# Kernel optimization log

Hardware: AMD Instinct MI355X
Metric: run time of the kernel (lower is better)

Reference implementation:

```python
import jax, jax.numpy as jnp
import numpy as np

DIM = 768
HEADS = 12
HEAD_DIM = DIM // HEADS
SCALE = HEAD_DIM ** -0.5


def setup_inputs() -> dict:
    key = jax.random.key(0)
    ks = jax.random.split(key, 7)
    B, N, C = 4, 1024, DIM
    s = 0.02
    return {
        "x": jax.random.normal(ks[0], (B, N, C), dtype=jnp.float32),
        "attn_mask": jax.random.normal(ks[1], (B, N, N), dtype=jnp.float32) * 0.1,
        "w_qkv": jax.random.normal(ks[2], (3 * C, C), dtype=jnp.float32) * s,
        "w_proj": jax.random.normal(ks[3], (C, C), dtype=jnp.float32) * s,
        "b_proj": jnp.zeros((C,), dtype=jnp.float32),
        "w_pre": jax.random.normal(ks[4], (HEADS, HEADS), dtype=jnp.float32) * 0.2,
        "w_post": jax.random.normal(ks[5], (HEADS, HEADS), dtype=jnp.float32) * 0.2,
    }


def reference(x, attn_mask, w_qkv, w_proj, b_proj, w_pre, w_post):
    B, N, C = x.shape
    H, D = HEADS, HEAD_DIM
    qkv = (x @ w_qkv.T).reshape(B, N, 3, H, D)
    q, k, v = jnp.moveaxis(qkv, 2, 0)          # each [B, N, H, D]
    q = q.transpose(0, 2, 1, 3)                # [B, H, N, D]
    k = k.transpose(0, 2, 1, 3)
    v = v.transpose(0, 2, 1, 3)
    attn = jnp.einsum("bhnd,bhmd->bhnm", q, k) * SCALE
    attn = attn + attn_mask[:, None, :, :]
    # talking-heads pre-softmax mixing: Linear over head axis (y = x @ W.T)
    attn = jnp.einsum("bhnm,gh->bgnm", attn, w_pre)
    attn = jax.nn.softmax(attn, axis=-1)
    # talking-heads post-softmax mixing
    attn = jnp.einsum("bhnm,gh->bgnm", attn, w_post)
    out = jnp.einsum("bhnm,bhmd->bhnd", attn, v)   # [B, H, N, D]
    out = out.transpose(0, 2, 1, 3).reshape(B, N, C)
    return out @ w_proj.T + b_proj
```

## Files before the change

### kernel.cpp

```cpp
#include <hip/hip_runtime.h>
#include <hip/hip_bf16.h>

typedef __attribute__((ext_vector_type(8))) short bf16x8;
typedef __attribute__((ext_vector_type(4))) float f32x4;
typedef unsigned short u16;

#define ATT_SCALE 0.125f

__device__ __forceinline__ u16 f2bf(float f){
  __hip_bfloat16 h = __float2bfloat16(f);
  return *reinterpret_cast<u16*>(&h);
}
__device__ __forceinline__ float bf2f(u16 u){
  __hip_bfloat16 h;
  *reinterpret_cast<u16*>(&h) = u;
  return __bfloat162float(h);
}

__global__ __launch_bounds__(256) void cvt_kernel(const float* __restrict__ src,
                                                  u16* __restrict__ dst, int n4){
  int i = blockIdx.x*256 + threadIdx.x;
  if (i < n4){
    float4 v = reinterpret_cast<const float4*>(src)[i];
    ushort4 o;
    o.x = f2bf(v.x); o.y = f2bf(v.y); o.z = f2bf(v.z); o.w = f2bf(v.w);
    reinterpret_cast<ushort4*>(dst)[i] = o;
  }
}

template<int BM, int BN, int MODE>
__global__ __launch_bounds__(256) void gemm_bt(
    const u16* __restrict__ A, const u16* __restrict__ B,
    void* __restrict__ C0, void* __restrict__ C1, void* __restrict__ C2,
    const float* __restrict__ bias,
    int M, int N, int K, int lda, int ldb, long sA, long sB, long sC)
{
  constexpr int BK = 32, LDT = 40;
  __shared__ u16 As[BM*LDT];
  __shared__ u16 Bs[BN*LDT];
  const int z = blockIdx.z;
  const u16* Ab = A + (long)z * sA;
  const u16* Bb = B + (long)z * sB;
  const int bm = blockIdx.x * BM, bn = blockIdx.y * BN;
  const int tid = threadIdx.x, lane = tid & 63, wv = tid >> 6;
  constexpr int WM = BM/2, WN = BN/2, FM = WM/16, FN = WN/16;
  const int wm = (wv >> 1) * WM, wn = (wv & 1) * WN;
  const int quad = lane >> 4, cl = lane & 15;
  f32x4 acc[FM][FN];
  #pragma unroll
  for (int i=0;i<FM;i++)
    #pragma unroll
    for (int j=0;j<FN;j++){ f32x4 zr = {0.f,0.f,0.f,0.f}; acc[i][j] = zr; }
  constexpr int AIT = (BM*BK)/(8*256);
  constexpr int BIT = (BN*BK)/(8*256);

  for (int kb = 0; kb < K; kb += BK){
    __syncthreads();
    #pragma unroll
    for (int sL=0; sL<AIT; sL++){
      int e = tid + sL*256, r = e >> 2, c8 = (e & 3) * 8;
      *reinterpret_cast<float4*>(&As[r*LDT + c8]) =
        *reinterpret_cast<const float4*>(Ab + (long)(bm + r)*lda + kb + c8);
    }
    #pragma unroll
    for (int sL=0; sL<BIT; sL++){
      int e = tid + sL*256, r = e >> 2, c8 = (e & 3) * 8;
      *reinterpret_cast<float4*>(&Bs[r*LDT + c8]) =
        *reinterpret_cast<const float4*>(Bb + (long)(bn + r)*ldb + kb + c8);
    }
    __syncthreads();
    bf16x8 af[FM], bfr[FN];
    #pragma unroll
    for (int i=0;i<FM;i++)
      af[i] = *reinterpret_cast<const bf16x8*>(&As[(wm + i*16 + cl)*LDT + quad*8]);
    #pragma unroll
    for (int j=0;j<FN;j++)
      bfr[j] = *reinterpret_cast<const bf16x8*>(&Bs[(wn + j*16 + cl)*LDT + quad*8]);
    #pragma unroll
    for (int i=0;i<FM;i++)
      #pragma unroll
      for (int j=0;j<FN;j++)
        acc[i][j] = __builtin_amdgcn_mfma_f32_16x16x32_bf16(af[i], bfr[j], acc[i][j], 0, 0, 0);
  }

  #pragma unroll
  for (int i=0;i<FM;i++)
  #pragma unroll
  for (int j=0;j<FN;j++)
  #pragma unroll
  for (int r=0;r<4;r++){
    int gm = bm + wm + i*16 + quad*4 + r;
    int gn = bn + wn + j*16 + cl;
    float v = acc[i][j][r];
    if (MODE == 0){
      int b_ = gm >> 10, n_ = gm & 1023;
      int t3 = (gn >= 1536) ? 2 : ((gn >= 768) ? 1 : 0);
      int rem = gn - t3*768;
      int h = rem >> 6, d = rem & 63;
      u16 hv = f2bf(v);
      if (t3 == 0)      ((u16*)C0)[((long)((b_*12 + h)*1024 + n_))*64 + d] = hv;
      else if (t3 == 1) ((u16*)C1)[((long)((b_*12 + h)*1024 + n_))*64 + d] = hv;
      else              ((u16*)C2)[((long)((b_*12 + h)*64 + d))*1024 + n_] = hv;
    } else if (MODE == 1){
      ((u16*)C0)[(long)z*sC + (long)gm*N + gn] = f2bf(v);
    } else if (MODE == 2){
      int b_ = z / 12, h = z - b_*12;
      ((u16*)C0)[((long)((b_*1024 + gm)*12 + h))*64 + gn] = f2bf(v);
    } else {
      ((float*)C0)[(long)gm*N + gn] = v + bias[gn];
    }
  }
}

__global__ __launch_bounds__(256) void mix_kernel(
    u16* __restrict__ S, const float* __restrict__ mask,
    const float* __restrict__ w_pre, const float* __restrict__ w_post)
{
  const int bid = blockIdx.x;
  const int b = bid >> 10, n = bid & 1023;
  const int t = threadIdx.x, wv = t >> 6, lane = t & 63;
  const int m0 = t * 4;

  float s[12][4];
  #pragma unroll
  for (int h=0; h<12; h++){
    ushort4 v = *reinterpret_cast<const ushort4*>(
        S + ((long)((b*12 + h)*1024 + n))*1024 + m0);
    s[h][0]=bf2f(v.x); s[h][1]=bf2f(v.y); s[h][2]=bf2f(v.z); s[h][3]=bf2f(v.w);
  }
  float4 mk = *reinterpret_cast<const float4*>(mask + ((long)(b*1024 + n))*1024 + m0);
  float mkv[4] = {mk.x, mk.y, mk.z, mk.w};

  float smix[12][4];
  #pragma unroll
  for (int g=0; g<12; g++){
    float rs = 0.f;
    #pragma unroll
    for (int h=0; h<12; h++) rs += w_pre[g*12 + h];
    #pragma unroll
    for (int mi=0; mi<4; mi++) smix[g][mi] = rs * mkv[mi];
    #pragma unroll
    for (int h=0; h<12; h++){
      float w = w_pre[g*12 + h] * ATT_SCALE;
      #pragma unroll
      for (int mi=0; mi<4; mi++) smix[g][mi] += w * s[h][mi];
    }
  }

  __shared__ float redA[12][4];
  __shared__ float redB[12][4];
  float Mg[12];
  #pragma unroll
  for (int g=0; g<12; g++){
    float v = fmaxf(fmaxf(smix[g][0], smix[g][1]), fmaxf(smix[g][2], smix[g][3]));
    #pragma unroll
    for (int off=32; off>0; off>>=1) v = fmaxf(v, __shfl_xor(v, off));
    if (lane == 0) redA[g][wv] = v;
  }
  __syncthreads();
  #pragma unroll
  for (int g=0; g<12; g++)
    Mg[g] = fmaxf(fmaxf(redA[g][0], redA[g][1]), fmaxf(redA[g][2], redA[g][3]));

  #pragma unroll
  for (int g=0; g<12; g++){
    float sum = 0.f;
    #pragma unroll
    for (int mi=0; mi<4; mi++){
      float e = __expf(smix[g][mi] - Mg[g]);
      smix[g][mi] = e; sum += e;
    }
    #pragma unroll
    for (int off=32; off>0; off>>=1) sum += __shfl_xor(sum, off);
    if (lane == 0) redB[g][wv] = sum;
  }
  __syncthreads();
  #pragma unroll
  for (int g=0; g<12; g++){
    float L = redB[g][0] + redB[g][1] + redB[g][2] + redB[g][3];
    float inv = 1.f / L;
    #pragma unroll
    for (int mi=0; mi<4; mi++) smix[g][mi] *= inv;
  }

  #pragma unroll
  for (int h=0; h<12; h++){
    float o0=0.f,o1=0.f,o2=0.f,o3=0.f;
    #pragma unroll
    for (int g=0; g<12; g++){
      float w = w_post[h*12 + g];
      o0 += w*smix[g][0]; o1 += w*smix[g][1]; o2 += w*smix[g][2]; o3 += w*smix[g][3];
    }
    ushort4 st; st.x=f2bf(o0); st.y=f2bf(o1); st.z=f2bf(o2); st.w=f2bf(o3);
    *reinterpret_cast<ushort4*>(S + ((long)((b*12 + h)*1024 + n))*1024 + m0) = st;
  }
}

extern "C" void kernel_launch(void* const* d_in, const int* in_sizes, int n_in,
                              void* d_out, int out_size, void* d_ws, size_t ws_size,
                              hipStream_t stream)
{
  const float* x      = (const float*)d_in[0];
  const float* mask   = (const float*)d_in[1];
  const float* w_qkv  = (const float*)d_in[2];
  const float* w_proj = (const float*)d_in[3];
  const float* b_proj = (const float*)d_in[4];
  const float* w_pre  = (const float*)d_in[5];
  const float* w_post = (const float*)d_in[6];
  float* out = (float*)d_out;

  u16* xb     = (u16*)d_ws;
  u16* wqkvb  = xb     + 4096l*768;
  u16* wprojb = wqkvb  + 2304l*768;
  u16* Qb     = wprojb + 768l*768;
  u16* Kb     = Qb     + 48l*1024*64;
  u16* Vtb    = Kb     + 48l*1024*64;
  u16* tmpb   = Vtb    + 48l*1024*64;
  u16* Sb     = tmpb   + 4096l*768;
  size_t need = ((size_t)(Sb - xb) + 48ul*1024*1024) * sizeof(u16);
  if (ws_size < need) return;

  cvt_kernel<<<(4096*768/4 + 255)/256, 256, 0, stream>>>(x,      xb,     4096*768/4);
  cvt_kernel<<<(2304*768/4 + 255)/256, 256, 0, stream>>>(w_qkv,  wqkvb,  2304*768/4);
  cvt_kernel<<<(768*768/4  + 255)/256, 256, 0, stream>>>(w_proj, wprojb, 768*768/4);

  dim3 gq(4096/128, 2304/128, 1);
  gemm_bt<128,128,0><<<gq, 256, 0, stream>>>(xb, wqkvb, Qb, Kb, Vtb, nullptr,
      4096, 2304, 768, 768, 768, 0, 0, 0);

  dim3 gs(1024/128, 1024/128, 48);
  gemm_bt<128,128,1><<<gs, 256, 0, stream>>>(Qb, Kb, Sb, nullptr, nullptr, nullptr,
      1024, 1024, 64, 64, 64, 1024l*64, 1024l*64, 1024l*1024);

  mix_kernel<<<4096, 256, 0, stream>>>(Sb, mask, w_pre, w_post);

  dim3 gp(1024/128, 1, 48);
  gemm_bt<128,64,2><<<gp, 256, 0, stream>>>(Sb, Vtb, tmpb, nullptr, nullptr, nullptr,
      1024, 64, 1024, 1024, 1024, 1024l*1024, 64l*1024, 0);

  dim3 go(4096/128, 768/128, 1);
  gemm_bt<128,128,3><<<go, 256, 0, stream>>>(tmpb, wprojb, out, nullptr, nullptr, b_proj,
      4096, 768, 768, 768, 768, 0, 0, 0);
}
```

Before: 275.3 us.

## Shrink mix kernel to one wave per row, fold scale into weights, merge conversions

The talking-heads mix kernel now runs one 64-thread wave per query row, with each lane handling 16 columns through 16-byte loads and stores. This removes the LDS reductions and __syncthreads, leaving only wave shuffles. The attention scale is folded into the Q part of w_qkv during bf16 conversion, and the three conversion launches are merged into one kernel. The risks are heavy register pressure from the 12x16 accumulator array and fewer threads per block, which could lower occupancy or cause spills.

```diff
diff --git a/kernel.cpp b/kernel.cpp
--- a/kernel.cpp
+++ b/kernel.cpp
@@ -2,10 +2,9 @@
 #include <hip/hip_bf16.h>
 
 typedef __attribute__((ext_vector_type(8))) short bf16x8;
+typedef __attribute__((ext_vector_type(8))) short s16x8;
 typedef __attribute__((ext_vector_type(4))) float f32x4;
 typedef unsigned short u16;
-
-#define ATT_SCALE 0.125f
 
 __device__ __forceinline__ u16 f2bf(float f){
   __hip_bfloat16 h = __float2bfloat16(f);
@@ -17,15 +16,24 @@
   return __bfloat162float(h);
 }
 
-__global__ __launch_bounds__(256) void cvt_kernel(const float* __restrict__ src,
-                                                  u16* __restrict__ dst, int n4){
+__global__ __launch_bounds__(256) void cvt3_kernel(
+    const float* __restrict__ s0, u16* __restrict__ d0, int n0,
+    const float* __restrict__ s1, u16* __restrict__ d1, int n1,
+    const float* __restrict__ s2, u16* __restrict__ d2, int n2)
+{
   int i = blockIdx.x*256 + threadIdx.x;
-  if (i < n4){
-    float4 v = reinterpret_cast<const float4*>(src)[i];
-    ushort4 o;
-    o.x = f2bf(v.x); o.y = f2bf(v.y); o.z = f2bf(v.z); o.w = f2bf(v.w);
-    reinterpret_cast<ushort4*>(dst)[i] = o;
-  }
+  const float* s; u16* d; int idx; float sc = 1.f;
+  if (i < n0){ s = s0; d = d0; idx = i; }
+  else if (i < n0 + n1){
+    idx = i - n0; s = s1; d = d1;
+    if (idx < 768*192) sc = 0.125f;
+  } else if (i < n0 + n1 + n2){
+    idx = i - n0 - n1; s = s2; d = d2;
+  } else return;
+  float4 v = reinterpret_cast<const float4*>(s)[idx];
+  ushort4 o;
+  o.x = f2bf(v.x*sc); o.y = f2bf(v.y*sc); o.z = f2bf(v.z*sc); o.w = f2bf(v.w*sc);
+  reinterpret_cast<ushort4*>(d)[idx] = o;
 }
 
 template<int BM, int BN, int MODE>
@@ -112,87 +120,127 @@
   }
 }
 
-__global__ __launch_bounds__(256) void mix_kernel(
+__global__ __launch_bounds__(64, 2) void mix_kernel(
     u16* __restrict__ S, const float* __restrict__ mask,
     const float* __restrict__ w_pre, const float* __restrict__ w_post)
 {
   const int bid = blockIdx.x;
   const int b = bid >> 10, n = bid & 1023;
-  const int t = threadIdx.x, wv = t >> 6, lane = t & 63;
-  const int m0 = t * 4;
-
-  float s[12][4];
+  const int l = threadIdx.x;
+  const long base0 = (((long)(b*12))*1024 + n) * 1024;
+  const int off0 = l*8, off1 = 512 + l*8;
+
+  float smix[12][16];
+
   #pragma unroll
   for (int h=0; h<12; h++){
-    ushort4 v = *reinterpret_cast<const ushort4*>(
-        S + ((long)((b*12 + h)*1024 + n))*1024 + m0);
-    s[h][0]=bf2f(v.x); s[h][1]=bf2f(v.y); s[h][2]=bf2f(v.z); s[h][3]=bf2f(v.w);
-  }
-  float4 mk = *reinterpret_cast<const float4*>(mask + ((long)(b*1024 + n))*1024 + m0);
-  float mkv[4] = {mk.x, mk.y, mk.z, mk.w};
-
-  float smix[12][4];
-  #pragma unroll
-  for (int g=0; g<12; g++){
-    float rs = 0.f;
-    #pragma unroll
-    for (int h=0; h<12; h++) rs += w_pre[g*12 + h];
-    #pragma unroll
-    for (int mi=0; mi<4; mi++) smix[g][mi] = rs * mkv[mi];
-    #pragma unroll
-    for (int h=0; h<12; h++){
-      float w = w_pre[g*12 + h] * ATT_SCALE;
-      #pragma unroll
-      for (int mi=0; mi<4; mi++) smix[g][mi] += w * s[h][mi];
-    }
-  }
-
-  __shared__ float redA[12][4];
-  __shared__ float redB[12][4];
-  float Mg[12];
-  #pragma unroll
-  for (int g=0; g<12; g++){
-    float v = fmaxf(fmaxf(smix[g][0], smix[g][1]), fmaxf(smix[g][2], smix[g][3]));
-    #pragma unroll
-    for (int off=32; off>0; off>>=1) v = fmaxf(v, __shfl_xor(v, off));
-    if (lane == 0) redA[g][wv] = v;
-  }
-  __syncthreads();
-  #pragma unroll
-  for (int g=0; g<12; g++)
-    Mg[g] = fmaxf(fmaxf(redA[g][0], redA[g][1]), fmaxf(redA[g][2], redA[g][3]));
-
-  #pragma unroll
-  for (int g=0; g<12; g++){
+    const u16* sr = S + base0 + (long)h*1024*1024;
+    bf16x8 v0 = *reinterpret_cast<const bf16x8*>(sr + off0);
+    bf16x8 v1 = *reinterpret_cast<const bf16x8*>(sr + off1);
+    float sv[16];
+    #pragma unroll
+    for (int j=0;j<8;j++){ sv[j] = bf2f((u16)v0[j]); sv[8+j] = bf2f((u16)v1[j]); }
+    if (h == 0){
+      #pragma unroll
+      for (int g=0;g<12;g++){
+        float w = w_pre[g*12];
+        #pragma unroll
+        for (int mi=0;mi<16;mi++) smix[g][mi] = w * sv[mi];
+      }
+    } else {
+      #pragma unroll
+      for (int g=0;g<12;g++){
+        float w = w_pre[g*12 + h];
+        #pragma unroll
+        for (int mi=0;mi<16;mi++) smix[g][mi] += w * sv[mi];
+      }
+    }
+  }
+
+  {
+    const float* mr = mask + ((long)(b*1024 + n))*1024;
+    float mk[16];
+    float4 a0 = *reinterpret_cast<const float4*>(mr + off0);
+    float4 a1 = *reinterpret_cast<const float4*>(mr + off0 + 4);
+    float4 b0 = *reinterpret_cast<const float4*>(mr + off1);
+    float4 b1 = *reinterpret_cast<const float4*>(mr + off1 + 4);
+    mk[0]=a0.x; mk[1]=a0.y; mk[2]=a0.z; mk[3]=a0.w;
+    mk[4]=a1.x; mk[5]=a1.y; mk[6]=a1.z; mk[7]=a1.w;
+    mk[8]=b0.x; mk[9]=b0.y; mk[10]=b0.z; mk[11]=b0.w;
+    mk[12]=b1.x; mk[13]=b1.y; mk[14]=b1.z; mk[15]=b1.w;
+    #pragma unroll
+    for (int g=0;g<12;g++){
+      float rs = 0.f;
+      #pragma unroll
+      for (int h=0;h<12;h++) rs += w_pre[g*12 + h];
+      #pragma unroll
+      for (int mi=0;mi<16;mi++) smix[g][mi] += rs * mk[mi];
+    }
+  }
+
+  float M[12];
+  #pragma unroll
+  for (int g=0;g<12;g++){
+    float a = fmaxf(smix[g][0], smix[g][1]);
+    float c = fmaxf(smix[g][2], smix[g][3]);
+    float e = fmaxf(smix[g][4], smix[g][5]);
+    float f = fmaxf(smix[g][6], smix[g][7]);
+    float a2 = fmaxf(smix[g][8], smix[g][9]);
+    float c2 = fmaxf(smix[g][10], smix[g][11]);
+    float e2 = fmaxf(smix[g][12], smix[g][13]);
+    float f2 = fmaxf(smix[g][14], smix[g][15]);
+    M[g] = fmaxf(fmaxf(fmaxf(a,c), fmaxf(e,f)), fmaxf(fmaxf(a2,c2), fmaxf(e2,f2)));
+  }
+  #pragma unroll
+  for (int off=32; off>0; off>>=1)
+    #pragma unroll
+    for (int g=0;g<12;g++) M[g] = fmaxf(M[g], __shfl_xor(M[g], off));
+
+  float L[12];
+  #pragma unroll
+  for (int g=0;g<12;g++){
     float sum = 0.f;
     #pragma unroll
-    for (int mi=0; mi<4; mi++){
-      float e = __expf(smix[g][mi] - Mg[g]);
+    for (int mi=0;mi<16;mi++){
+      float e = __expf(smix[g][mi] - M[g]);
       smix[g][mi] = e; sum += e;
     }
-    #pragma unroll
-    for (int off=32; off>0; off>>=1) sum += __shfl_xor(sum, off);
-    if (lane == 0) redB[g][wv] = sum;
-  }
-  __syncthreads();
-  #pragma unroll
-  for (int g=0; g<12; g++){
-    float L = redB[g][0] + redB[g][1] + redB[g][2] + redB[g][3];
-    float inv = 1.f / L;
-    #pragma unroll
-    for (int mi=0; mi<4; mi++) smix[g][mi] *= inv;
+    L[g] = sum;
+  }
+  #pragma unroll
+  for (int off=32; off>0; off>>=1)
+    #pragma unroll
+    for (int g=0;g<12;g++) L[g] += __shfl_xor(L[g], off);
+  #pragma unroll
+  for (int g=0;g<12;g++){
+    float inv = 1.0f / L[g];
+    #pragma unroll
+    for (int mi=0;mi<16;mi++) smix[g][mi] *= inv;
   }
 
   #pragma unroll
   for (int h=0; h<12; h++){
-    float o0=0.f,o1=0.f,o2=0.f,o3=0.f;
-    #pragma unroll
-    for (int g=0; g<12; g++){
+    float o[16];
+    {
+      float w = w_post[h*12];
+      #pragma unroll
+      for (int mi=0;mi<16;mi++) o[mi] = w * smix[0][mi];
+    }
+    #pragma unroll
+    for (int g=1;g<12;g++){
       float w = w_post[h*12 + g];
-      o0 += w*smix[g][0]; o1 += w*smix[g][1]; o2 += w*smix[g][2]; o3 += w*smix[g][3];
-    }
-    ushort4 st; st.x=f2bf(o0); st.y=f2bf(o1); st.z=f2bf(o2); st.w=f2bf(o3);
-    *reinterpret_cast<ushort4*>(S + ((long)((b*12 + h)*1024 + n))*1024 + m0) = st;
+      #pragma unroll
+      for (int mi=0;mi<16;mi++) o[mi] += w * smix[g][mi];
+    }
+    s16x8 st0, st1;
+    #pragma unroll
+    for (int j=0;j<8;j++){
+      st0[j] = (short)f2bf(o[j]);
+      st1[j] = (short)f2bf(o[8+j]);
+    }
+    u16* orow = S + base0 + (long)h*1024*1024;
+    *reinterpret_cast<s16x8*>(orow + off0) = st0;
+    *reinterpret_cast<s16x8*>(orow + off1) = st1;
   }
 }
 
@@ -220,9 +268,9 @@
   size_t need = ((size_t)(Sb - xb) + 48ul*1024*1024) * sizeof(u16);
   if (ws_size < need) return;
 
-  cvt_kernel<<<(4096*768/4 + 255)/256, 256, 0, stream>>>(x,      xb,     4096*768/4);
-  cvt_kernel<<<(2304*768/4 + 255)/256, 256, 0, stream>>>(w_qkv,  wqkvb,  2304*768/4);
-  cvt_kernel<<<(768*768/4  + 255)/256, 256, 0, stream>>>(w_proj, wprojb, 768*768/4);
+  const int n0 = 4096*768/4, n1 = 2304*768/4, n2 = 768*768/4;
+  cvt3_kernel<<<(n0+n1+n2 + 255)/256, 256, 0, stream>>>(x, xb, n0, w_qkv, wqkvb, n1,
+                                                        w_proj, wprojb, n2);
 
   dim3 gq(4096/128, 2304/128, 1);
   gemm_bt<128,128,0><<<gq, 256, 0, stream>>>(xb, wqkvb, Qb, Kb, Vtb, nullptr,
@@ -232,7 +280,7 @@
   gemm_bt<128,128,1><<<gs, 256, 0, stream>>>(Qb, Kb, Sb, nullptr, nullptr, nullptr,
       1024, 1024, 64, 64, 64, 1024l*64, 1024l*64, 1024l*1024);
 
-  mix_kernel<<<4096, 256, 0, stream>>>(Sb, mask, w_pre, w_post);
+  mix_kernel<<<4096, 64, 0, stream>>>(Sb, mask, w_pre, w_post);
 
   dim3 gp(1024/128, 1, 48);
   gemm_bt<128,64,2><<<gp, 256, 0, stream>>>(Sb, Vtb, tmpb, nullptr, nullptr, nullptr,
```

Result: slower. 293.4 us (+6.6%).
